# Kernel optimization log

Hardware: AMD Instinct MI355X
Metric: run time of the kernel (lower is better)

Reference implementation:

```python
import jax, jax.numpy as jnp
import numpy as np


def _area2d(a, b, c):
    # signed parallelogram area; broadcasts (b may be a [S,S,2] grid)
    return (b[..., 0] - a[..., 0]) * (c[..., 1] - a[..., 1]) - (b[..., 1] - a[..., 1]) * (c[..., 0] - a[..., 0])


def _lookup_table(size):
    # matches torch: meshgrid(ij) of linspace(-1,1), stack [xx,yy], rot90
    lin = jnp.linspace(-1.0, 1.0, size, dtype=jnp.float32)
    xx, yy = jnp.meshgrid(lin, lin, indexing='ij')
    t = jnp.stack([xx, yy], axis=-1)
    return jnp.rot90(t, 1)  # [S,S,2] screen-space (x,y) per pixel


def _grid_sample(img, grid):
    # bilinear, zeros padding, align_corners=True (old 4-arg ATen grid_sampler_2d)
    C, H, W = img.shape
    x = (grid[..., 0] + 1.0) * 0.5 * (W - 1)
    y = (grid[..., 1] + 1.0) * 0.5 * (H - 1)
    x0 = jnp.floor(x)
    y0 = jnp.floor(y)
    wx = x - x0
    wy = y - y0

    def gather(ix, iy):
        inb = (ix >= 0) & (ix <= W - 1) & (iy >= 0) & (iy <= H - 1)
        ii = jnp.clip(ix, 0, W - 1).astype(jnp.int32)
        jj = jnp.clip(iy, 0, H - 1).astype(jnp.int32)
        return img[:, jj, ii] * inb[None].astype(img.dtype)  # [C,h,w]

    v00 = gather(x0, y0)
    v10 = gather(x0 + 1, y0)
    v01 = gather(x0, y0 + 1)
    v11 = gather(x0 + 1, y0 + 1)
    return (v00 * ((1 - wx) * (1 - wy))[None] + v10 * (wx * (1 - wy))[None]
            + v01 * ((1 - wx) * wy)[None] + v11 * (wx * wy)[None])


def _render(tris, uvs, uvmap, size):
    S = size
    pts = _lookup_table(S)            # [S,S,2]
    uvs_v = uvs * 2.0 - 1.0           # module maps uvs from [0,1] to [-1,1]
    zmin = jnp.min(tris.reshape(-1, 3), axis=0)[2]
    zbuf0 = jnp.full((S, S), zmin, dtype=tris.dtype)
    res0 = jnp.zeros((4, S, S), dtype=tris.dtype)

    def step(carry, tu):
        zbuf, res = carry
        tri, uv = tu                  # tri [3,3], uv [3,2]
        t2 = tri[:, :2]
        w = _area2d(t2[0], t2[1], t2[2])
        valid = w >= 1e-9             # degenerate triangle -> skipped (masked out)
        ws = jnp.where(valid, w, 1.0)
        pAB = _area2d(t2[1], pts, t2[0])
        pCB = _area2d(t2[2], pts, t2[1])
        pCA = _area2d(t2[0], pts, t2[2])
        inside = (jnp.maximum(pAB, 0.0) * jnp.maximum(pCB, 0.0) * jnp.maximum(pCA, 0.0) > 0) & valid
        w1 = pCB / ws
        w2 = pCA / ws
        w3 = 1.0 - w1 - w2
        pts3d = w1[..., None] * tri[0] + w2[..., None] * tri[1] + w3[..., None] * tri[2]  # [S,S,3]
        z = pts3d[..., 2]
        zmsk = z >= zbuf
        ptsUV = w1[..., None] * uv[0] + w2[..., None] * uv[1] + w3[..., None] * uv[2]      # [S,S,2]
        rgb = _grid_sample(uvmap, ptsUV)[:3]  # [3,S,S]
        rmsk = inside & zmsk
        zbuf = jnp.where(rmsk, z, zbuf)
        res = jnp.concatenate([jnp.where(rmsk[None], rgb, res[:3]),
                               jnp.where(rmsk, 1.0, res[3])[None]], axis=0)
        return (zbuf, res), None

    (_, res), _ = jax.lax.scan(step, (zbuf0, res0), (tris, uvs_v))
    return res


def setup_inputs():
    key = jax.random.key(0)
    k1, k2, k3 = jax.random.split(key, 3)
    tris = jax.random.uniform(k1, (256, 3, 3), jnp.float32, -1.0, 1.0)
    uvs = jax.random.uniform(k2, (256, 3, 2), jnp.float32)
    uvmap = jax.random.uniform(k3, (3, 1024, 1024), jnp.float32)
    return {"tris": tris, "uvs": uvs, "uvmap": uvmap, "size": 256}


def reference(tris, uvs, uvmap, size):
    return _render(tris, uvs, uvmap, size)
```

## Files before the change

### kernel.cpp

```cpp
#include <hip/hip_runtime.h>


#define S 256
#define TMAX 256
#define NC 8
#define BT 1024
#define HALF 128
#define MARGIN 0.02f

__global__ __launch_bounds__(BT) void render_kernel(
    const float* __restrict__ tris,
    const float* __restrict__ uvs,
    const float* __restrict__ uvmap,
    float* __restrict__ out,
    int T)
{
#pragma clang fp contract(off)
    __shared__ float4 sd[TMAX][4];
    __shared__ int    list[TMAX];
    __shared__ unsigned long long masks[4];
    __shared__ float  zpart[4];
    __shared__ float4 cand[NC][HALF];

    const int tid  = threadIdx.x;
    const int bid  = blockIdx.x;
    const int row  = bid >> 1;
    const int half = bid & 1;
    const int j    = half * HALF + (tid & (HALF - 1));
    const int c    = tid >> 7;

    const float px = (float)(-1.0 + (double)j * (2.0 / 255.0));
    const float py = (float)(-1.0 + (double)(S - 1 - row) * (2.0 / 255.0));
    const float pxlo = (float)(-1.0 + (double)(half * HALF) * (2.0 / 255.0));
    const float pxhi = (float)(-1.0 + (double)(half * HALF + HALF - 1) * (2.0 / 255.0));

    bool keep = false;
    float zl = 3.0e38f;
    if (tid < TMAX && tid < T) {
        const float* p = tris + tid * 9;
        float Ax = p[0], Ay = p[1], Az = p[2];
        float Bx = p[3], By = p[4], Bz = p[5];
        float Cx = p[6], Cy = p[7], Cz = p[8];
        float w = (Bx - Ax) * (Cy - Ay) - (By - Ay) * (Cx - Ax);
        bool valid = (w >= 1e-9f);
        sd[tid][0] = make_float4(Bx, By, Ay - By, Ax - Bx);
        sd[tid][1] = make_float4(Cx, Cy, By - Cy, Bx - Cx);
        sd[tid][2] = make_float4(Ax, Ay, Cy - Ay, Cx - Ax);
        sd[tid][3] = make_float4(valid ? w : 1.0f, Az, Bz, Cz);
        zl = fminf(Az, fminf(Bz, Cz));
        float ymn = fminf(Ay, fminf(By, Cy));
        float ymx = fmaxf(Ay, fmaxf(By, Cy));
        float xmn = fminf(Ax, fminf(Bx, Cx));
        float xmx = fmaxf(Ax, fmaxf(Bx, Cx));
        keep = valid && (py >= ymn - MARGIN) && (py <= ymx + MARGIN)
                     && (pxhi >= xmn - MARGIN) && (pxlo <= xmx + MARGIN);
    }
    unsigned long long m = __ballot(keep);
    if (tid < TMAX) {
        float zw = zl;
        #pragma unroll
        for (int o = 32; o > 0; o >>= 1) zw = fminf(zw, __shfl_xor(zw, o, 64));
        if ((tid & 63) == 0) { masks[tid >> 6] = m; zpart[tid >> 6] = zw; }
    }
    __syncthreads();

    int n0 = __popcll(masks[0]);
    int n1 = __popcll(masks[1]);
    int n2 = __popcll(masks[2]);
    int n3 = __popcll(masks[3]);
    const int nlive = n0 + n1 + n2 + n3;
    const float zmin = fminf(fminf(zpart[0], zpart[1]), fminf(zpart[2], zpart[3]));

    if (tid < TMAX && keep) {
        int lane = tid & 63;
        int wv   = tid >> 6;
        int off  = (wv > 0 ? n0 : 0) + (wv > 1 ? n1 : 0) + (wv > 2 ? n2 : 0);
        int pos  = off + __popcll(masks[wv] & ((1ull << lane) - 1ull));
        list[pos] = tid;
    }
    __syncthreads();

    const int cs = (nlive + NC - 1) / NC;
    const int tb = c * cs;
    const int te = (tb + cs < nlive) ? (tb + cs) : nlive;

    float zcur = zmin;
    int win = -1;
    float w1w = 0.0f, w2w = 0.0f;

    for (int it = tb; it < te; ++it) {
        int tt = list[it];
        float4 r0 = sd[tt][0];
        float4 r1 = sd[tt][1];
        float4 r2 = sd[tt][2];
        float4 r3 = sd[tt][3];
        float pAB = (px - r0.x) * r0.z - (py - r0.y) * r0.w;
        float pCB = (px - r1.x) * r1.z - (py - r1.y) * r1.w;
        float pCA = (px - r2.x) * r2.z - (py - r2.y) * r2.w;
        float prod = fmaxf(pAB, 0.0f) * fmaxf(pCB, 0.0f) * fmaxf(pCA, 0.0f);
        if (prod > 0.0f) {
            float w1 = pCB / r3.x;
            float w2 = pCA / r3.x;
            float w3 = (1.0f - w1) - w2;
            float z = (w1 * r3.y + w2 * r3.z) + w3 * r3.w;
            if (z >= zcur) { zcur = z; win = tt; w1w = w1; w2w = w2; }
        }
    }
    cand[c][tid & (HALF - 1)] = make_float4(zcur, w1w, w2w, (float)win);
    __syncthreads();

    if (tid < HALF) {
        float zb = 0.0f, w1 = 0.0f, w2 = 0.0f;
        int w = -1;
        #pragma unroll
        for (int k = 0; k < NC; ++k) {
            float4 ck = cand[k][tid];
            int cw = (int)ck.w;
            if (cw >= 0 && (w < 0 || ck.x >= zb)) {
                zb = ck.x; w1 = ck.y; w2 = ck.z; w = cw;
            }
        }

        float r = 0.0f, g = 0.0f, b = 0.0f, a = 0.0f;
        if (w >= 0) {
            a = 1.0f;
            float w3 = (1.0f - w1) - w2;
            const float* q = uvs + w * 6;
            float u0x = q[0] * 2.0f - 1.0f, u0y = q[1] * 2.0f - 1.0f;
            float u1x = q[2] * 2.0f - 1.0f, u1y = q[3] * 2.0f - 1.0f;
            float u2x = q[4] * 2.0f - 1.0f, u2y = q[5] * 2.0f - 1.0f;
            float ux = (w1 * u0x + w2 * u1x) + w3 * u2x;
            float uy = (w1 * u0y + w2 * u1y) + w3 * u2y;
            float X = ((ux + 1.0f) * 0.5f) * 1023.0f;
            float Y = ((uy + 1.0f) * 0.5f) * 1023.0f;
            float x0 = floorf(X), y0 = floorf(Y);
            float wx = X - x0, wy = Y - y0;
            float w00 = (1.0f - wx) * (1.0f - wy);
            float w10 = wx * (1.0f - wy);
            float w01 = (1.0f - wx) * wy;
            float w11 = wx * wy;
            float xs1 = x0 + 1.0f, ys1 = y0 + 1.0f;
            bool xin0 = (x0  >= 0.0f) && (x0  <= 1023.0f);
            bool xin1 = (xs1 >= 0.0f) && (xs1 <= 1023.0f);
            bool yin0 = (y0  >= 0.0f) && (y0  <= 1023.0f);
            bool yin1 = (ys1 >= 0.0f) && (ys1 <= 1023.0f);
            int xi0 = (int)fminf(fmaxf(x0,  0.0f), 1023.0f);
            int xi1 = (int)fminf(fmaxf(xs1, 0.0f), 1023.0f);
            int yi0 = (int)fminf(fmaxf(y0,  0.0f), 1023.0f);
            int yi1 = (int)fminf(fmaxf(ys1, 0.0f), 1023.0f);
            float acc[3];
            #pragma unroll
            for (int ch = 0; ch < 3; ++ch) {
                const float* img = uvmap + ch * (1024 * 1024);
                float v00 = (xin0 && yin0) ? img[yi0 * 1024 + xi0] : 0.0f;
                float v10 = (xin1 && yin0) ? img[yi0 * 1024 + xi1] : 0.0f;
                float v01 = (xin0 && yin1) ? img[yi1 * 1024 + xi0] : 0.0f;
                float v11 = (xin1 && yin1) ? img[yi1 * 1024 + xi1] : 0.0f;
                acc[ch] = ((v00 * w00 + v10 * w10) + v01 * w01) + v11 * w11;
            }
            r = acc[0]; g = acc[1]; b = acc[2];
        }

        const int base = row * S + j;
        out[0 * S * S + base] = r;
        out[1 * S * S + base] = g;
        out[2 * S * S + base] = b;
        out[3 * S * S + base] = a;
    }
}

extern "C" void kernel_launch(void* const* d_in, const int* in_sizes, int n_in,
                              void* d_out, int out_size, void* d_ws, size_t ws_size,
                              hipStream_t stream) {
    const float* tris  = (const float*)d_in[0];
    const float* uvs   = (const float*)d_in[1];
    const float* uvmap = (const float*)d_in[2];
    float* out = (float*)d_out;
    int T = in_sizes[0] / 9;
    if (T > TMAX) T = TMAX;
    render_kernel<<<dim3(2 * S), dim3(BT), 0, stream>>>(tris, uvs, uvmap, out, T);
}
```

Before: 75.95 us.

## Halve block size, merge per-chunk candidates with packed 64-bit atomicMax

```diff
diff --git a/kernel.cpp b/kernel.cpp
--- a/kernel.cpp
+++ b/kernel.cpp
@@ -3,12 +3,12 @@
 
 #define S 256
 #define TMAX 256
-#define NC 8
-#define BT 1024
+#define NC 4
+#define BT 512
 #define HALF 128
 #define MARGIN 0.02f
 
-__global__ __launch_bounds__(BT) void render_kernel(
+__global__ __launch_bounds__(BT, 4) void render_kernel(
     const float* __restrict__ tris,
     const float* __restrict__ uvs,
     const float* __restrict__ uvmap,
@@ -17,10 +17,11 @@
 {
 #pragma clang fp contract(off)
     __shared__ float4 sd[TMAX][4];
+    __shared__ float  suv[TMAX * 6];
     __shared__ int    list[TMAX];
     __shared__ unsigned long long masks[4];
     __shared__ float  zpart[4];
-    __shared__ float4 cand[NC][HALF];
+    __shared__ unsigned long long pix[HALF];
 
     const int tid  = threadIdx.x;
     const int bid  = blockIdx.x;
@@ -36,24 +37,29 @@
 
     bool keep = false;
     float zl = 3.0e38f;
-    if (tid < TMAX && tid < T) {
-        const float* p = tris + tid * 9;
-        float Ax = p[0], Ay = p[1], Az = p[2];
-        float Bx = p[3], By = p[4], Bz = p[5];
-        float Cx = p[6], Cy = p[7], Cz = p[8];
-        float w = (Bx - Ax) * (Cy - Ay) - (By - Ay) * (Cx - Ax);
-        bool valid = (w >= 1e-9f);
-        sd[tid][0] = make_float4(Bx, By, Ay - By, Ax - Bx);
-        sd[tid][1] = make_float4(Cx, Cy, By - Cy, Bx - Cx);
-        sd[tid][2] = make_float4(Ax, Ay, Cy - Ay, Cx - Ax);
-        sd[tid][3] = make_float4(valid ? w : 1.0f, Az, Bz, Cz);
-        zl = fminf(Az, fminf(Bz, Cz));
-        float ymn = fminf(Ay, fminf(By, Cy));
-        float ymx = fmaxf(Ay, fmaxf(By, Cy));
-        float xmn = fminf(Ax, fminf(Bx, Cx));
-        float xmx = fmaxf(Ax, fmaxf(Bx, Cx));
-        keep = valid && (py >= ymn - MARGIN) && (py <= ymx + MARGIN)
-                     && (pxhi >= xmn - MARGIN) && (pxlo <= xmx + MARGIN);
+    if (tid < TMAX) {
+        if (tid < T) {
+            const float* p = tris + tid * 9;
+            float Ax = p[0], Ay = p[1], Az = p[2];
+            float Bx = p[3], By = p[4], Bz = p[5];
+            float Cx = p[6], Cy = p[7], Cz = p[8];
+            float w = (Bx - Ax) * (Cy - Ay) - (By - Ay) * (Cx - Ax);
+            bool valid = (w >= 1e-9f);
+            sd[tid][0] = make_float4(Bx, By, Ay - By, Ax - Bx);
+            sd[tid][1] = make_float4(Cx, Cy, By - Cy, Bx - Cx);
+            sd[tid][2] = make_float4(Ax, Ay, Cy - Ay, Cx - Ax);
+            sd[tid][3] = make_float4(valid ? w : 1.0f, Az, Bz, Cz);
+            zl = fminf(Az, fminf(Bz, Cz));
+            float ymn = fminf(Ay, fminf(By, Cy));
+            float ymx = fmaxf(Ay, fmaxf(By, Cy));
+            float xmn = fminf(Ax, fminf(Bx, Cx));
+            float xmx = fmaxf(Ax, fmaxf(Bx, Cx));
+            keep = valid && (py >= ymn - MARGIN) && (py <= ymx + MARGIN)
+                         && (pxhi >= xmn - MARGIN) && (pxlo <= xmx + MARGIN);
+        }
+    } else {
+        for (int i = tid - TMAX; i < T * 6; i += BT - TMAX)
+            suv[i] = uvs[i] * 2.0f - 1.0f;
     }
     unsigned long long m = __ballot(keep);
     if (tid < TMAX) {
@@ -78,6 +84,7 @@
         int pos  = off + __popcll(masks[wv] & ((1ull << lane) - 1ull));
         list[pos] = tid;
     }
+    if (tid < HALF) pix[tid] = 0ull;
     __syncthreads();
 
     const int cs = (nlive + NC - 1) / NC;
@@ -86,7 +93,6 @@
 
     float zcur = zmin;
     int win = -1;
-    float w1w = 0.0f, w2w = 0.0f;
 
     for (int it = tb; it < te; ++it) {
         int tt = list[it];
@@ -103,34 +109,35 @@
             float w2 = pCA / r3.x;
             float w3 = (1.0f - w1) - w2;
             float z = (w1 * r3.y + w2 * r3.z) + w3 * r3.w;
-            if (z >= zcur) { zcur = z; win = tt; w1w = w1; w2w = w2; }
+            if (z >= zcur) { zcur = z; win = tt; }
         }
     }
-    cand[c][tid & (HALF - 1)] = make_float4(zcur, w1w, w2w, (float)win);
+    if (win >= 0) {
+        unsigned k = __float_as_uint(zcur);
+        k = (k & 0x80000000u) ? ~k : (k | 0x80000000u);
+        unsigned long long key =
+            ((unsigned long long)k << 32) | (unsigned)(win + 1);
+        atomicMax(&pix[tid & (HALF - 1)], key);
+    }
     __syncthreads();
 
     if (tid < HALF) {
-        float zb = 0.0f, w1 = 0.0f, w2 = 0.0f;
-        int w = -1;
-        #pragma unroll
-        for (int k = 0; k < NC; ++k) {
-            float4 ck = cand[k][tid];
-            int cw = (int)ck.w;
-            if (cw >= 0 && (w < 0 || ck.x >= zb)) {
-                zb = ck.x; w1 = ck.y; w2 = ck.z; w = cw;
-            }
-        }
-
+        unsigned long long key = pix[tid];
         float r = 0.0f, g = 0.0f, b = 0.0f, a = 0.0f;
-        if (w >= 0) {
+        if (key) {
+            int w = (int)(key & 0xffffffffu) - 1;
             a = 1.0f;
+            float4 r1 = sd[w][1];
+            float4 r2 = sd[w][2];
+            float4 r3 = sd[w][3];
+            float pCB = (px - r1.x) * r1.z - (py - r1.y) * r1.w;
+            float pCA = (px - r2.x) * r2.z - (py - r2.y) * r2.w;
+            float w1 = pCB / r3.x;
+            float w2 = pCA / r3.x;
             float w3 = (1.0f - w1) - w2;
-            const float* q = uvs + w * 6;
-            float u0x = q[0] * 2.0f - 1.0f, u0y = q[1] * 2.0f - 1.0f;
-            float u1x = q[2] * 2.0f - 1.0f, u1y = q[3] * 2.0f - 1.0f;
-            float u2x = q[4] * 2.0f - 1.0f, u2y = q[5] * 2.0f - 1.0f;
-            float ux = (w1 * u0x + w2 * u1x) + w3 * u2x;
-            float uy = (w1 * u0y + w2 * u1y) + w3 * u2y;
+            const float* q = &suv[w * 6];
+            float ux = (w1 * q[0] + w2 * q[2]) + w3 * q[4];
+            float uy = (w1 * q[1] + w2 * q[3]) + w3 * q[5];
             float X = ((ux + 1.0f) * 0.5f) * 1023.0f;
             float Y = ((uy + 1.0f) * 0.5f) * 1023.0f;
             float x0 = floorf(X), y0 = floorf(Y);
```

Measured after the change: 76.04 us. Within noise of the previous version (+0.1%).
